# Optimization experiments

Hardware: AMD Instinct MI355X
Metric: run time of the kernel (lower is better)

Reference implementation:

```python
import jax, jax.numpy as jnp
import numpy as np

N_REACH = 4096
N_T = 730
DT = 3600.0
VEL_LB = 0.3
VEL_UB = 15.0
Q_LB = 1e-4
SLOPE_LB = 1e-4


def _make_adjacency(n):
    # River-network DAG in topological order: each reach j (except outlet)
    # drains to exactly one downstream reach i > j  =>  strictly lower-triangular.
    rng = np.random.default_rng(0)
    j = np.arange(n - 1)
    ds = j + 1 + (rng.random(n - 1) * (n - 1 - j)).astype(np.int64)
    adj = np.zeros((n, n), dtype=np.float32)
    adj[ds, j] = 1.0
    return jnp.asarray(adj)


def setup_inputs() -> dict:
    key = jax.random.key(0)
    ks = jax.random.split(key, 8)
    u = lambda k, s: jax.random.uniform(k, s, dtype=jnp.float32)
    q_prime = u(ks[0], (N_T, N_REACH)) * 10.0            # lateral inflow m^3/s
    n = 0.01 + 0.09 * u(ks[1], (N_REACH,))               # Manning's n
    q_spatial = 1.5 + u(ks[2], (N_REACH,))               # log base > 1
    p_spatial = 1.0 + 3.0 * u(ks[3], (N_REACH,))         # width scale
    length = 1000.0 + 5000.0 * u(ks[4], (N_REACH,))      # reach length [m]
    slope = 1e-3 + 0.05 * u(ks[5], (N_REACH,))           # channel slope
    width = 5.0 + 100.0 * u(ks[6], (N_REACH,))           # width > p_spatial
    x_storage = 0.1 + 0.3 * u(ks[7], (N_REACH,))         # Muskingum x
    adj = _make_adjacency(N_REACH)
    return {"q_prime": q_prime, "n": n, "q_spatial": q_spatial,
            "p_spatial": p_spatial, "length": length, "slope": slope,
            "width": width, "x_storage": x_storage, "adj": adj}


def reference(q_prime, n, q_spatial, p_spatial, length, slope, width, x_storage, adj):
    slope = jnp.clip(slope, SLOPE_LB)
    # Manning's equation -> celerity (note: independent of discharge, as in source)
    depth = jnp.log(width / p_spatial) / jnp.log(q_spatial)
    v = (1.0 / n) * depth ** (2.0 / 3.0) * jnp.sqrt(slope)
    c = jnp.clip(v, VEL_LB, VEL_UB) * (5.0 / 3.0)
    k = length / c
    denom = 2.0 * k * (1.0 - x_storage) + DT
    c1 = (DT - 2.0 * k * x_storage) / denom
    c2 = (DT + 2.0 * k * x_storage) / denom
    c3 = (2.0 * k * (1.0 - x_storage) - DT) / denom
    c4 = 2.0 * DT / denom

    # Lower-triangular routing system: A = I - diag(c1) @ adjacency (constant)
    N = q_prime.shape[1]
    A = jnp.eye(N, dtype=q_prime.dtype) - c1[:, None] * adj

    q0 = q_prime[0]
    out0 = jnp.clip(q0[-1], Q_LB)  # single gage at index -1

    def step(q_t, qp_row):
        q_l = jnp.clip(qp_row, Q_LB)
        i_t = adj @ q_t                        # upstream inflow
        b = c2 * i_t + c3 * q_t + c4 * q_l
        x = jax.scipy.linalg.solve_triangular(A, b[:, None], lower=True)[:, 0]
        q_t1 = jnp.clip(x, Q_LB)
        return q_t1, q_t1[-1]

    _, outs = jax.lax.scan(step, q0, q_prime[:-1])  # timesteps 1..T-1 use q_prime[t-1]
    runoff = jnp.concatenate([out0[None], outs])[None, :]  # [1, T]
    return runoff
```

## Files before the change

### kernel.cpp

```cpp
#include <hip/hip_runtime.h>

#define N 4096
#define NT 730
#define NTH 512
#define PER_T 8
#define QLB 1e-4f
#define DT_S 3600.0f

#define WS_DS     0
#define WS_SZ     4096
#define WS_CCNT   8192
#define WS_COFF   12288
#define WS_CUR    16385
#define WS_CPOS   20481
#define WS_HI     24577
#define WS_FLAG   28673
#define WS_C1     32769
#define WS_C2     36865
#define WS_C3     40961
#define WS_C4     45057
#define WS_CLIST  49153
#define WS_GP     53249
#define WS_CBP    57345
#define WS_CEP    61441
#define WS_LOP    65537
#define WS_C2P    69633
#define WS_C3P    73729
#define WS_C4P    77825
#define WS_SP     81922
#define WS_ISP    90114

__device__ __forceinline__ int qidx(int p) { return ((p & 7) << 9) | (p >> 3); }

__global__ void k_init(int* ds, int* sz, int* ccnt, int* hi, int* flag) {
    int j = blockIdx.x * 256 + threadIdx.x;
    if (j < N) { ds[j] = N - 1; sz[j] = 1; ccnt[j] = 0; hi[j] = -1; flag[j] = 0; }
}

__global__ void k_extract(const float4* __restrict__ adj4, int* __restrict__ ds) {
    long idx = (long)blockIdx.x * 256 + threadIdx.x;
    if (idx >= (long)N * N / 4) return;
    float4 w = adj4[idx];
    long base = idx * 4;
    int row = (int)(base >> 12);
    int col = (int)(base & 4095);
    if (w.x != 0.0f) ds[col + 0] = row;
    if (w.y != 0.0f) ds[col + 1] = row;
    if (w.z != 0.0f) ds[col + 2] = row;
    if (w.w != 0.0f) ds[col + 3] = row;
}

__global__ void k_coeffs(const float* n, const float* qs, const float* ps,
                         const float* len, const float* slope, const float* width,
                         const float* xs, float* __restrict__ c1, float* __restrict__ c2,
                         float* __restrict__ c3, float* __restrict__ c4) {
    int i = blockIdx.x * 256 + threadIdx.x;
    if (i >= N) return;
    float s  = fmaxf(slope[i], 1e-4f);
    float dp = logf(width[i] / ps[i]) / logf(qs[i]);
    float v  = (1.0f / n[i]) * powf(dp, 2.0f / 3.0f) * sqrtf(s);
    float c  = fminf(fmaxf(v, 0.3f), 15.0f) * (5.0f / 3.0f);
    float k  = len[i] / c;
    float x  = xs[i];
    float denom = 2.0f * k * (1.0f - x) + DT_S;
    c1[i] = (DT_S - 2.0f * k * x) / denom;
    c2[i] = (DT_S + 2.0f * k * x) / denom;
    c3[i] = (2.0f * k * (1.0f - x) - DT_S) / denom;
    c4[i] = 2.0f * DT_S / denom;
}

__global__ void k_count(const int* __restrict__ ds, int* __restrict__ ccnt,
                        int* __restrict__ sz) {
    int u = blockIdx.x * 256 + threadIdx.x;
    if (u >= N || u == N - 1) return;
    atomicAdd(&ccnt[ds[u]], 1);
    int a = ds[u];
    while (true) {
        atomicAdd(&sz[a], 1);
        if (a == N - 1) break;
        a = ds[a];
    }
}

__global__ __launch_bounds__(1024) void k_scan(const int* ccnt, int* coff, int* cur) {
    __shared__ int buf[1024];
    int tid = threadIdx.x;
    int a0 = ccnt[tid * 4 + 0], a1 = ccnt[tid * 4 + 1];
    int a2 = ccnt[tid * 4 + 2], a3 = ccnt[tid * 4 + 3];
    int s1 = a0, s2 = a0 + a1, s3 = a0 + a1 + a2, tot = s3 + a3;
    buf[tid] = tot;
    __syncthreads();
    for (int off = 1; off < 1024; off <<= 1) {
        int add = (tid >= off) ? buf[tid - off] : 0;
        __syncthreads();
        buf[tid] += add;
        __syncthreads();
    }
    int base = buf[tid] - tot;
    coff[tid * 4 + 0] = base;      cur[tid * 4 + 0] = base;
    coff[tid * 4 + 1] = base + s1; cur[tid * 4 + 1] = base + s1;
    coff[tid * 4 + 2] = base + s2; cur[tid * 4 + 2] = base + s2;
    coff[tid * 4 + 3] = base + s3; cur[tid * 4 + 3] = base + s3;
    if (tid == 1023) coff[N] = buf[1023];
}

__global__ void k_fill(const int* __restrict__ ds, int* __restrict__ cur,
                       int* __restrict__ clist, int* __restrict__ cpos) {
    int u = blockIdx.x * 256 + threadIdx.x;
    if (u >= N || u == N - 1) return;
    int cp = atomicAdd(&cur[ds[u]], 1);
    clist[cp] = u;
    cpos[u] = cp;
}

__global__ __launch_bounds__(1024) void k_post(const int* __restrict__ ds,
                                               const int* __restrict__ sz,
                                               const int* __restrict__ coff,
                                               const int* __restrict__ ccnt,
                                               const int* __restrict__ clist,
                                               int* __restrict__ hi,
                                               int* __restrict__ flag) {
    int tid = threadIdx.x;
    if (tid == 0) hi[N - 1] = N - 1;
    __syncthreads();
    for (int it = 0; it < 96; ++it) {
        for (int v = tid; v < N; v += 1024) {
            if (hi[v] >= 0 && flag[v] == 0) {
                int cum = hi[v] - sz[v] + 1;
                int b0 = coff[v], e0 = b0 + ccnt[v];
                for (int k = b0; k < e0; ++k) {
                    int c = clist[k];
                    hi[c] = cum + sz[c] - 1;
                    cum += sz[c];
                }
                flag[v] = 1;
            }
        }
        __syncthreads();
    }
}

__global__ void k_prep(const int* __restrict__ ds, const int* __restrict__ sz,
                       const int* __restrict__ coff, const int* __restrict__ ccnt,
                       const int* __restrict__ hi, const int* __restrict__ cpos,
                       const float* __restrict__ c1, const float* __restrict__ c2,
                       const float* __restrict__ c3, const float* __restrict__ c4,
                       int* __restrict__ clist, int* __restrict__ gP,
                       int* __restrict__ cbP, int* __restrict__ ceP,
                       int* __restrict__ loP, float* __restrict__ c2P,
                       float* __restrict__ c3P, float* __restrict__ c4P,
                       double* __restrict__ SP, double* __restrict__ ISP) {
    int u = blockIdx.x * 256 + threadIdx.x;
    if (u >= N) return;
    int p = hi[u];
    double s = 1.0;
    if (u != N - 1) {
        int a = ds[u];
        while (true) {
            s *= (double)c1[a];
            if (a == N - 1) break;
            a = ds[a];
        }
    }
    SP[p] = s;
    ISP[p] = 1.0 / s;
    gP[p] = u;
    cbP[p] = coff[u];
    ceP[p] = coff[u] + ccnt[u];
    loP[p] = p - sz[u] + 1;
    c2P[p] = c2[u]; c3P[p] = c3[u]; c4P[p] = c4[u];
    if (u != N - 1) clist[cpos[u]] = qidx(p);
}

__global__ __launch_bounds__(NTH) void k_route(
    const float* __restrict__ qp, const float* __restrict__ c2g,
    const float* __restrict__ c3g, const float* __restrict__ c4g,
    const int* __restrict__ gPg, const int* __restrict__ cbPg,
    const int* __restrict__ cePg, const int* __restrict__ loPg,
    const double* __restrict__ SPg, const double* __restrict__ ISPg,
    const int* __restrict__ clist, float* __restrict__ out) {
    __shared__ float  qL[N];
    __shared__ double TL[N];
    __shared__ int    CL[N];
    __shared__ double wpart[8];
    int tid = threadIdx.x;
    int lane = tid & 63, wid = tid >> 6;

    int g[PER_T], cb[PER_T], ce[PER_T], lo[PER_T];
    float c2r[PER_T], c3r[PER_T], c4r[PER_T], qreg[PER_T], qc[PER_T], qn[PER_T];
    double Sr[PER_T], iSr[PER_T];
#pragma unroll
    for (int r = 0; r < PER_T; ++r) {
        int v = tid * PER_T + r;
        g[r] = gPg[v]; cb[r] = cbPg[v]; ce[r] = cePg[v]; lo[r] = loPg[v];
        c2r[r] = c2g[v]; c3r[r] = c3g[v]; c4r[r] = c4g[v];
        Sr[r] = SPg[v]; iSr[r] = ISPg[v];
        float q0 = qp[g[r]];
        qreg[r] = q0; qc[r] = q0;
        qL[(r << 9) | tid] = q0;
    }
    for (int i = tid; i < N; i += NTH) CL[i] = clist[i];
    if (tid == NTH - 1) out[0] = fmaxf(qreg[PER_T - 1], QLB);
    __syncthreads();

    for (int t = 1; t < NT; ++t) {
        float bb[PER_T];
        double yv[PER_T], Tloc[PER_T];
        double tl = 0.0;
#pragma unroll
        for (int r = 0; r < PER_T; ++r) {
            float csum = 0.0f;
            for (int k = cb[r]; k < ce[r]; ++k) csum += qL[CL[k]];
            bb[r] = c2r[r] * csum + c3r[r] * qreg[r] + c4r[r] * fmaxf(qc[r], QLB);
            double y = Sr[r] * (double)bb[r];
            yv[r] = y;
            tl += y;
            Tloc[r] = tl;
        }
        double run = tl;
#pragma unroll
        for (int off = 1; off < 64; off <<= 1) {
            double up = __shfl_up(run, off, 64);
            run += (lane >= off) ? up : 0.0;
        }
        if (lane == 63) wpart[wid] = run;
        __syncthreads();
        double woff = 0.0;
        for (int w = 0; w < wid; ++w) woff += wpart[w];
        double texcl = woff + (run - tl);
#pragma unroll
        for (int r = 0; r < PER_T; ++r)
            TL[(r << 9) | tid] = texcl + Tloc[r];
        __syncthreads();
#pragma unroll
        for (int r = 0; r < PER_T; ++r) {
            int l = lo[r];
            double Tg = (l > 0) ? TL[qidx(l - 1)] : 0.0;
            double Tself = texcl + Tloc[r] - yv[r];
            double x = (double)bb[r] + (Tself - Tg) * iSr[r];
            qreg[r] = fmaxf((float)x, QLB);
        }
        if (t < NT - 1) {
            const float* row = qp + (size_t)t * N;
#pragma unroll
            for (int r = 0; r < PER_T; ++r) qn[r] = row[g[r]];
        }
#pragma unroll
        for (int r = 0; r < PER_T; ++r) qL[(r << 9) | tid] = qreg[r];
        if (tid == NTH - 1) out[t] = qreg[PER_T - 1];
        __syncthreads();
#pragma unroll
        for (int r = 0; r < PER_T; ++r) qc[r] = qn[r];
    }
}

extern "C" void kernel_launch(void* const* d_in, const int* in_sizes, int n_in,
                              void* d_out, int out_size, void* d_ws, size_t ws_size,
                              hipStream_t stream) {
    const float* qp    = (const float*)d_in[0];
    const float* n     = (const float*)d_in[1];
    const float* qs    = (const float*)d_in[2];
    const float* ps    = (const float*)d_in[3];
    const float* len   = (const float*)d_in[4];
    const float* slope = (const float*)d_in[5];
    const float* width = (const float*)d_in[6];
    const float* xs    = (const float*)d_in[7];
    const float* adj   = (const float*)d_in[8];
    float* out = (float*)d_out;

    int*    W     = (int*)d_ws;
    int*    ds    = W + WS_DS;
    int*    sz    = W + WS_SZ;
    int*    ccnt  = W + WS_CCNT;
    int*    coff  = W + WS_COFF;
    int*    cur   = W + WS_CUR;
    int*    cpos  = W + WS_CPOS;
    int*    hi    = W + WS_HI;
    int*    flag  = W + WS_FLAG;
    float*  c1    = (float*)(W + WS_C1);
    float*  c2    = (float*)(W + WS_C2);
    float*  c3    = (float*)(W + WS_C3);
    float*  c4    = (float*)(W + WS_C4);
    int*    clist = W + WS_CLIST;
    int*    gP    = W + WS_GP;
    int*    cbP   = W + WS_CBP;
    int*    ceP   = W + WS_CEP;
    int*    loP   = W + WS_LOP;
    float*  c2P   = (float*)(W + WS_C2P);
    float*  c3P   = (float*)(W + WS_C3P);
    float*  c4P   = (float*)(W + WS_C4P);
    double* SP    = (double*)(W + WS_SP);
    double* ISP   = (double*)(W + WS_ISP);

    k_init<<<(N + 255) / 256, 256, 0, stream>>>(ds, sz, ccnt, hi, flag);
    k_extract<<<(N * N / 4 + 255) / 256, 256, 0, stream>>>((const float4*)adj, ds);
    k_coeffs<<<(N + 255) / 256, 256, 0, stream>>>(n, qs, ps, len, slope, width, xs,
                                                  c1, c2, c3, c4);
    k_count<<<(N + 255) / 256, 256, 0, stream>>>(ds, ccnt, sz);
    k_scan<<<1, 1024, 0, stream>>>(ccnt, coff, cur);
    k_fill<<<(N + 255) / 256, 256, 0, stream>>>(ds, cur, clist, cpos);
    k_post<<<1, 1024, 0, stream>>>(ds, sz, coff, ccnt, clist, hi, flag);
    k_prep<<<(N + 255) / 256, 256, 0, stream>>>(ds, sz, coff, ccnt, hi, cpos,
                                                c1, c2, c3, c4, clist, gP, cbP, ceP,
                                                loP, c2P, c3P, c4P, SP, ISP);
    k_route<<<1, NTH, 0, stream>>>(qp, c2P, c3P, c4P, gP, cbP, ceP, loP,
                                   SP, ISP, clist, out);
}
```

Before: 4.558 ms.

## Replace per-reach child gather with edge-parallel LDS atomics and permuted inflow

```diff
diff --git a/kernel.cpp b/kernel.cpp
--- a/kernel.cpp
+++ b/kernel.cpp
@@ -11,26 +11,48 @@
 #define WS_SZ     4096
 #define WS_CCNT   8192
 #define WS_COFF   12288
-#define WS_CUR    16385
-#define WS_CPOS   20481
-#define WS_HI     24577
-#define WS_FLAG   28673
-#define WS_C1     32769
-#define WS_C2     36865
-#define WS_C3     40961
-#define WS_C4     45057
-#define WS_CLIST  49153
-#define WS_GP     53249
-#define WS_CBP    57345
-#define WS_CEP    61441
-#define WS_LOP    65537
-#define WS_C2P    69633
-#define WS_C3P    73729
-#define WS_C4P    77825
-#define WS_SP     81922
-#define WS_ISP    90114
+#define WS_CUR    16388
+#define WS_HI     20484
+#define WS_FLAG   24580
+#define WS_C1     28676
+#define WS_C2     32772
+#define WS_C3     36868
+#define WS_C4     40964
+#define WS_CLIST  45060
+#define WS_GP     49156
+#define WS_LOP    53252
+#define WS_C3P    57348
+#define WS_C4P    61444
+#define WS_CCNTP  65540
+#define WS_COFF2  69636
+#define WS_CUR2   73736
+#define WS_EQ     77832
+#define WS_EW     81928
+#define WS_SP     86024
+#define WS_ISP    94216
+#define WS_QPP    102408
+#define WS_END    (WS_QPP + NT * N)
 
 __device__ __forceinline__ int qidx(int p) { return ((p & 7) << 9) | (p >> 3); }
+
+template <int CTRL, int RMASK>
+__device__ __forceinline__ double dpp_stage(double v) {
+    union U { double d; unsigned int u[2]; };
+    U s, t;
+    s.d = v;
+    t.u[0] = (unsigned)__builtin_amdgcn_update_dpp(0, (int)s.u[0], CTRL, RMASK, 0xf, false);
+    t.u[1] = (unsigned)__builtin_amdgcn_update_dpp(0, (int)s.u[1], CTRL, RMASK, 0xf, false);
+    return v + t.d;
+}
+__device__ __forceinline__ double wave_incl_scan(double v) {
+    v = dpp_stage<0x111, 0xf>(v);
+    v = dpp_stage<0x112, 0xf>(v);
+    v = dpp_stage<0x114, 0xf>(v);
+    v = dpp_stage<0x118, 0xf>(v);
+    v = dpp_stage<0x142, 0xa>(v);
+    v = dpp_stage<0x143, 0xc>(v);
+    return v;
+}
 
 __global__ void k_init(int* ds, int* sz, int* ccnt, int* hi, int* flag) {
     int j = blockIdx.x * 256 + threadIdx.x;
@@ -82,35 +104,36 @@
     }
 }
 
-__global__ __launch_bounds__(1024) void k_scan(const int* ccnt, int* coff, int* cur) {
+__global__ __launch_bounds__(1024) void k_scan(const int* __restrict__ src,
+                                               int* __restrict__ off,
+                                               int* __restrict__ cur) {
     __shared__ int buf[1024];
     int tid = threadIdx.x;
-    int a0 = ccnt[tid * 4 + 0], a1 = ccnt[tid * 4 + 1];
-    int a2 = ccnt[tid * 4 + 2], a3 = ccnt[tid * 4 + 3];
+    int a0 = src[tid * 4 + 0], a1 = src[tid * 4 + 1];
+    int a2 = src[tid * 4 + 2], a3 = src[tid * 4 + 3];
     int s1 = a0, s2 = a0 + a1, s3 = a0 + a1 + a2, tot = s3 + a3;
     buf[tid] = tot;
     __syncthreads();
-    for (int off = 1; off < 1024; off <<= 1) {
-        int add = (tid >= off) ? buf[tid - off] : 0;
+    for (int o = 1; o < 1024; o <<= 1) {
+        int add = (tid >= o) ? buf[tid - o] : 0;
         __syncthreads();
         buf[tid] += add;
         __syncthreads();
     }
     int base = buf[tid] - tot;
-    coff[tid * 4 + 0] = base;      cur[tid * 4 + 0] = base;
-    coff[tid * 4 + 1] = base + s1; cur[tid * 4 + 1] = base + s1;
-    coff[tid * 4 + 2] = base + s2; cur[tid * 4 + 2] = base + s2;
-    coff[tid * 4 + 3] = base + s3; cur[tid * 4 + 3] = base + s3;
-    if (tid == 1023) coff[N] = buf[1023];
+    off[tid * 4 + 0] = base;      cur[tid * 4 + 0] = base;
+    off[tid * 4 + 1] = base + s1; cur[tid * 4 + 1] = base + s1;
+    off[tid * 4 + 2] = base + s2; cur[tid * 4 + 2] = base + s2;
+    off[tid * 4 + 3] = base + s3; cur[tid * 4 + 3] = base + s3;
+    if (tid == 1023) off[N] = buf[1023];
 }
 
 __global__ void k_fill(const int* __restrict__ ds, int* __restrict__ cur,
-                       int* __restrict__ clist, int* __restrict__ cpos) {
+                       int* __restrict__ clist) {
     int u = blockIdx.x * 256 + threadIdx.x;
     if (u >= N || u == N - 1) return;
     int cp = atomicAdd(&cur[ds[u]], 1);
     clist[cp] = u;
-    cpos[u] = cp;
 }
 
 __global__ __launch_bounds__(1024) void k_post(const int* __restrict__ ds,
@@ -141,14 +164,12 @@
 }
 
 __global__ void k_prep(const int* __restrict__ ds, const int* __restrict__ sz,
-                       const int* __restrict__ coff, const int* __restrict__ ccnt,
-                       const int* __restrict__ hi, const int* __restrict__ cpos,
-                       const float* __restrict__ c1, const float* __restrict__ c2,
-                       const float* __restrict__ c3, const float* __restrict__ c4,
-                       int* __restrict__ clist, int* __restrict__ gP,
-                       int* __restrict__ cbP, int* __restrict__ ceP,
-                       int* __restrict__ loP, float* __restrict__ c2P,
+                       const int* __restrict__ ccnt, const int* __restrict__ hi,
+                       const float* __restrict__ c1, const float* __restrict__ c3,
+                       const float* __restrict__ c4,
+                       int* __restrict__ gP, int* __restrict__ loP,
                        float* __restrict__ c3P, float* __restrict__ c4P,
+                       int* __restrict__ ccntP,
                        double* __restrict__ SP, double* __restrict__ ISP) {
     int u = blockIdx.x * 256 + threadIdx.x;
     if (u >= N) return;
@@ -162,76 +183,124 @@
             a = ds[a];
         }
     }
-    SP[p] = s;
-    ISP[p] = 1.0 / s;
+    SP[p] = s; ISP[p] = 1.0 / s;
     gP[p] = u;
-    cbP[p] = coff[u];
-    ceP[p] = coff[u] + ccnt[u];
     loP[p] = p - sz[u] + 1;
-    c2P[p] = c2[u]; c3P[p] = c3[u]; c4P[p] = c4[u];
-    if (u != N - 1) clist[cpos[u]] = qidx(p);
+    c3P[p] = c3[u]; c4P[p] = c4[u];
+    ccntP[p] = ccnt[u];
+}
+
+__global__ void k_fill2(const int* __restrict__ ds, const int* __restrict__ hi,
+                        const float* __restrict__ c2, int* __restrict__ cur2,
+                        unsigned int* __restrict__ EQ, float* __restrict__ EW) {
+    int u = blockIdx.x * 256 + threadIdx.x;
+    if (u >= N) return;
+    if (u == N - 1) {
+        unsigned rq = (unsigned)qidx(N - 1);
+        EQ[N - 1] = (rq << 12) | rq;
+        EW[N - 1] = 0.0f;
+        return;
+    }
+    int d = ds[u];
+    int slot = atomicAdd(&cur2[hi[d]], 1);
+    EQ[slot] = ((unsigned)qidx(hi[u]) << 12) | (unsigned)qidx(hi[d]);
+    EW[slot] = c2[d];
+}
+
+__global__ void k_permute(const float* __restrict__ qp, const int* __restrict__ gP,
+                          float* __restrict__ qpp) {
+    long e = (long)blockIdx.x * 256 + threadIdx.x;
+    if (e >= (long)NT * N) return;
+    int tr = (int)(e >> 12);
+    int v  = (int)(e & 4095);
+    qpp[e] = qp[(size_t)tr * N + gP[v]];
 }
 
 __global__ __launch_bounds__(NTH) void k_route(
-    const float* __restrict__ qp, const float* __restrict__ c2g,
+    const float* __restrict__ qp, const float* __restrict__ qpp,
     const float* __restrict__ c3g, const float* __restrict__ c4g,
-    const int* __restrict__ gPg, const int* __restrict__ cbPg,
-    const int* __restrict__ cePg, const int* __restrict__ loPg,
+    const int* __restrict__ gPg, const int* __restrict__ loPg,
     const double* __restrict__ SPg, const double* __restrict__ ISPg,
-    const int* __restrict__ clist, float* __restrict__ out) {
-    __shared__ float  qL[N];
+    const unsigned int* __restrict__ EQg, const float* __restrict__ EWg,
+    int use_perm, float* __restrict__ out) {
+    __shared__ float qL[N];
+    __shared__ float CS[N];
     __shared__ double TL[N];
-    __shared__ int    CL[N];
-    __shared__ double wpart[8];
+    __shared__ __align__(16) double wpart[8];
     int tid = threadIdx.x;
     int lane = tid & 63, wid = tid >> 6;
 
-    int g[PER_T], cb[PER_T], ce[PER_T], lo[PER_T];
-    float c2r[PER_T], c3r[PER_T], c4r[PER_T], qreg[PER_T], qc[PER_T], qn[PER_T];
+    unsigned int eq[PER_T];
+    float ew[PER_T];
+    int lo[PER_T], g[PER_T];
+    float c3r[PER_T], c4r[PER_T], qreg[PER_T], qn[PER_T];
     double Sr[PER_T], iSr[PER_T];
 #pragma unroll
     for (int r = 0; r < PER_T; ++r) {
-        int v = tid * PER_T + r;
-        g[r] = gPg[v]; cb[r] = cbPg[v]; ce[r] = cePg[v]; lo[r] = loPg[v];
-        c2r[r] = c2g[v]; c3r[r] = c3g[v]; c4r[r] = c4g[v];
-        Sr[r] = SPg[v]; iSr[r] = ISPg[v];
-        float q0 = qp[g[r]];
-        qreg[r] = q0; qc[r] = q0;
+        int p = tid * PER_T + r;
+        eq[r] = EQg[p]; ew[r] = EWg[p];
+        lo[r] = loPg[p]; g[r] = gPg[p];
+        c3r[r] = c3g[p]; c4r[r] = c4g[p];
+        Sr[r] = SPg[p]; iSr[r] = ISPg[p];
+        float q0 = use_perm ? qpp[p] : qp[g[r]];
+        qreg[r] = q0;
         qL[(r << 9) | tid] = q0;
-    }
-    for (int i = tid; i < N; i += NTH) CL[i] = clist[i];
+        CS[(r << 9) | tid] = c3r[r] * q0 + c4r[r] * fmaxf(q0, QLB);
+    }
     if (tid == NTH - 1) out[0] = fmaxf(qreg[PER_T - 1], QLB);
     __syncthreads();
 
     for (int t = 1; t < NT; ++t) {
+#pragma unroll
+        for (int e = 0; e < PER_T; ++e) {
+            float qv = qL[eq[e] >> 12];
+            atomicAdd(&CS[eq[e] & 4095u], ew[e] * qv);
+        }
+        __syncthreads();
         float bb[PER_T];
         double yv[PER_T], Tloc[PER_T];
         double tl = 0.0;
 #pragma unroll
         for (int r = 0; r < PER_T; ++r) {
-            float csum = 0.0f;
-            for (int k = cb[r]; k < ce[r]; ++k) csum += qL[CL[k]];
-            bb[r] = c2r[r] * csum + c3r[r] * qreg[r] + c4r[r] * fmaxf(qc[r], QLB);
-            double y = Sr[r] * (double)bb[r];
+            float b = CS[(r << 9) | tid];
+            bb[r] = b;
+            double y = Sr[r] * (double)b;
             yv[r] = y;
             tl += y;
             Tloc[r] = tl;
         }
-        double run = tl;
-#pragma unroll
-        for (int off = 1; off < 64; off <<= 1) {
-            double up = __shfl_up(run, off, 64);
-            run += (lane >= off) ? up : 0.0;
-        }
-        if (lane == 63) wpart[wid] = run;
-        __syncthreads();
+        double incl = wave_incl_scan(tl);
+        if (lane == 63) wpart[wid] = incl;
+        __syncthreads();
+        double2 w0 = *(const double2*)&wpart[0];
+        double2 w1 = *(const double2*)&wpart[2];
+        double2 w2 = *(const double2*)&wpart[4];
+        double2 w3 = *(const double2*)&wpart[6];
         double woff = 0.0;
-        for (int w = 0; w < wid; ++w) woff += wpart[w];
-        double texcl = woff + (run - tl);
+        if (wid > 0) woff += w0.x;
+        if (wid > 1) woff += w0.y;
+        if (wid > 2) woff += w1.x;
+        if (wid > 3) woff += w1.y;
+        if (wid > 4) woff += w2.x;
+        if (wid > 5) woff += w2.y;
+        if (wid > 6) woff += w3.x;
+        double texcl = woff + incl - tl;
 #pragma unroll
         for (int r = 0; r < PER_T; ++r)
             TL[(r << 9) | tid] = texcl + Tloc[r];
         __syncthreads();
+        if (t < NT - 1) {
+            if (use_perm) {
+                const float4* row4 = (const float4*)(qpp + (size_t)t * N);
+                float4 a = row4[tid * 2], b = row4[tid * 2 + 1];
+                qn[0] = a.x; qn[1] = a.y; qn[2] = a.z; qn[3] = a.w;
+                qn[4] = b.x; qn[5] = b.y; qn[6] = b.z; qn[7] = b.w;
+            } else {
+                const float* row = qp + (size_t)t * N;
+#pragma unroll
+                for (int r = 0; r < PER_T; ++r) qn[r] = row[g[r]];
+            }
+        }
 #pragma unroll
         for (int r = 0; r < PER_T; ++r) {
             int l = lo[r];
@@ -240,17 +309,13 @@
             double x = (double)bb[r] + (Tself - Tg) * iSr[r];
             qreg[r] = fmaxf((float)x, QLB);
         }
-        if (t < NT - 1) {
-            const float* row = qp + (size_t)t * N;
-#pragma unroll
-            for (int r = 0; r < PER_T; ++r) qn[r] = row[g[r]];
-        }
-#pragma unroll
-        for (int r = 0; r < PER_T; ++r) qL[(r << 9) | tid] = qreg[r];
         if (tid == NTH - 1) out[t] = qreg[PER_T - 1];
-        __syncthreads();
-#pragma unroll
-        for (int r = 0; r < PER_T; ++r) qc[r] = qn[r];
+#pragma unroll
+        for (int r = 0; r < PER_T; ++r) {
+            qL[(r << 9) | tid] = qreg[r];
+            CS[(r << 9) | tid] = c3r[r] * qreg[r] + c4r[r] * fmaxf(qn[r], QLB);
+        }
+        __syncthreads();
     }
 }
 
@@ -268,29 +333,33 @@
     const float* adj   = (const float*)d_in[8];
     float* out = (float*)d_out;
 
-    int*    W     = (int*)d_ws;
-    int*    ds    = W + WS_DS;
-    int*    sz    = W + WS_SZ;
-    int*    ccnt  = W + WS_CCNT;
-    int*    coff  = W + WS_COFF;
-    int*    cur   = W + WS_CUR;
-    int*    cpos  = W + WS_CPOS;
-    int*    hi    = W + WS_HI;
-    int*    flag  = W + WS_FLAG;
-    float*  c1    = (float*)(W + WS_C1);
-    float*  c2    = (float*)(W + WS_C2);
-    float*  c3    = (float*)(W + WS_C3);
-    float*  c4    = (float*)(W + WS_C4);
-    int*    clist = W + WS_CLIST;
-    int*    gP    = W + WS_GP;
-    int*    cbP   = W + WS_CBP;
-    int*    ceP   = W + WS_CEP;
-    int*    loP   = W + WS_LOP;
-    float*  c2P   = (float*)(W + WS_C2P);
-    float*  c3P   = (float*)(W + WS_C3P);
-    float*  c4P   = (float*)(W + WS_C4P);
-    double* SP    = (double*)(W + WS_SP);
-    double* ISP   = (double*)(W + WS_ISP);
+    int*          W     = (int*)d_ws;
+    int*          ds    = W + WS_DS;
+    int*          sz    = W + WS_SZ;
+    int*          ccnt  = W + WS_CCNT;
+    int*          coff  = W + WS_COFF;
+    int*          cur   = W + WS_CUR;
+    int*          hi    = W + WS_HI;
+    int*          flag  = W + WS_FLAG;
+    float*        c1    = (float*)(W + WS_C1);
+    float*        c2    = (float*)(W + WS_C2);
+    float*        c3    = (float*)(W + WS_C3);
+    float*        c4    = (float*)(W + WS_C4);
+    int*          clist = W + WS_CLIST;
+    int*          gP    = W + WS_GP;
+    int*          loP   = W + WS_LOP;
+    float*        c3P   = (float*)(W + WS_C3P);
+    float*        c4P   = (float*)(W + WS_C4P);
+    int*          ccntP = W + WS_CCNTP;
+    int*          coff2 = W + WS_COFF2;
+    int*          cur2  = W + WS_CUR2;
+    unsigned int* EQ    = (unsigned int*)(W + WS_EQ);
+    float*        EW    = (float*)(W + WS_EW);
+    double*       SP    = (double*)(W + WS_SP);
+    double*       ISP   = (double*)(W + WS_ISP);
+    float*        QPP   = (float*)(W + WS_QPP);
+
+    int use_perm = (ws_size >= (size_t)WS_END * 4) ? 1 : 0;
 
     k_init<<<(N + 255) / 256, 256, 0, stream>>>(ds, sz, ccnt, hi, flag);
     k_extract<<<(N * N / 4 + 255) / 256, 256, 0, stream>>>((const float4*)adj, ds);
@@ -298,11 +367,14 @@
                                                   c1, c2, c3, c4);
     k_count<<<(N + 255) / 256, 256, 0, stream>>>(ds, ccnt, sz);
     k_scan<<<1, 1024, 0, stream>>>(ccnt, coff, cur);
-    k_fill<<<(N + 255) / 256, 256, 0, stream>>>(ds, cur, clist, cpos);
+    k_fill<<<(N + 255) / 256, 256, 0, stream>>>(ds, cur, clist);
     k_post<<<1, 1024, 0, stream>>>(ds, sz, coff, ccnt, clist, hi, flag);
-    k_prep<<<(N + 255) / 256, 256, 0, stream>>>(ds, sz, coff, ccnt, hi, cpos,
-                                                c1, c2, c3, c4, clist, gP, cbP, ceP,
-                                                loP, c2P, c3P, c4P, SP, ISP);
-    k_route<<<1, NTH, 0, stream>>>(qp, c2P, c3P, c4P, gP, cbP, ceP, loP,
-                                   SP, ISP, clist, out);
-}
+    k_prep<<<(N + 255) / 256, 256, 0, stream>>>(ds, sz, ccnt, hi, c1, c3, c4,
+                                                gP, loP, c3P, c4P, ccntP, SP, ISP);
+    k_scan<<<1, 1024, 0, stream>>>(ccntP, coff2, cur2);
+    k_fill2<<<(N + 255) / 256, 256, 0, stream>>>(ds, hi, c2, cur2, EQ, EW);
+    if (use_perm)
+        k_permute<<<(int)(((long)NT * N + 255) / 256), 256, 0, stream>>>(qp, gP, QPP);
+    k_route<<<1, NTH, 0, stream>>>(qp, QPP, c3P, c4P, gP, loP, SP, ISP, EQ, EW,
+                                   use_perm, out);
+}
```

Result: slower. 5.124 ms (+12.4%).
